# Kernel tuning notes

Hardware: AMD Instinct MI355X
Metric: run time of the kernel (lower is better)

The kernel has to match this reference:

```python
import jax, jax.numpy as jnp
import numpy as np

N = 131072          # batch_size(64) * cycle_size(2048) total graph nodes
E = 2097152         # N * avg_degree(16) edges


def _gcn_block(x, edge_index, W_self, W_nbr, b):
    """GraphConv-style STGCN spatial block: self-transform + mean-aggregated
    neighbor transform over edge_index (gather -> segment-reduce -> scatter)."""
    src, dst = edge_index[0], edge_index[1]
    msg = jax.ops.segment_sum(x[src], dst, num_segments=N)            # [N, C_in]
    deg = jax.ops.segment_sum(jnp.ones((edge_index.shape[1],), x.dtype), dst,
                              num_segments=N)                          # [N]
    agg = msg / jnp.maximum(deg, 1.0)[:, None]
    return x @ W_self + agg @ W_nbr + b


def setup_inputs() -> dict:
    key = jax.random.key(0)
    ks = jax.random.split(key, 16)

    def lin(k, fan_in, fan_out):
        return jax.random.normal(k, (fan_in, fan_out), jnp.float32) / np.sqrt(fan_in)

    x = jax.random.normal(ks[0], (N, 16), jnp.float32)
    edge_index = jax.random.randint(ks[1], (2, E), 0, N)
    batch = jnp.zeros((N,), jnp.int64) if jax.config.jax_enable_x64 else jnp.zeros((N,), jnp.int32)

    return {
        "x": x,
        "edge_index": edge_index,
        "batch": batch,
        "W_lin": lin(ks[2], 16, 16),
        "b_lin": jnp.zeros((16,), jnp.float32),
        # block3: 16 -> 32
        "Ws3": lin(ks[3], 16, 32), "Wn3": lin(ks[4], 16, 32), "b3": jnp.zeros((32,), jnp.float32),
        # block2: 32 -> 64
        "Ws2": lin(ks[5], 32, 64), "Wn2": lin(ks[6], 32, 64), "b2": jnp.zeros((64,), jnp.float32),
        # block1: 64 -> 128
        "Ws1": lin(ks[7], 64, 128), "Wn1": lin(ks[8], 64, 128), "b1": jnp.zeros((128,), jnp.float32),
    }


def reference(x, edge_index, batch, W_lin, b_lin,
              Ws3, Wn3, b3, Ws2, Wn2, b2, Ws1, Wn1, b1):
    h = x @ W_lin + b_lin                                   # Linear(16,16)
    h = jax.nn.relu(_gcn_block(h, edge_index, Ws3, Wn3, b3))   # 16 -> 32
    h = jax.nn.relu(_gcn_block(h, edge_index, Ws2, Wn2, b2))   # 32 -> 64
    h = jax.nn.sigmoid(_gcn_block(h, edge_index, Ws1, Wn1, b1))  # 64 -> 128
    return h
```

## Files before the change

kernel.cpp:

```cpp
#include <hip/hip_runtime.h>
#include <cmath>


typedef __attribute__((ext_vector_type(8))) _Float16 half8;
typedef __attribute__((ext_vector_type(4))) float floatx4;

#define NBUCKET 512
#define BUCKET_SHIFT 8

__global__ __launch_bounds__(256) void bucket_hist_kernel(
    const int* __restrict__ dst, int* __restrict__ bcnt, int E, int EPB, int nblk) {
    __shared__ int lh[NBUCKET];
    for (int i = threadIdx.x; i < NBUCKET; i += 256) lh[i] = 0;
    __syncthreads();
    int base = blockIdx.x * EPB;
    int end  = min(base + EPB, E);
    for (int i = base + threadIdx.x; i < end; i += 256)
        atomicAdd(&lh[dst[i] >> BUCKET_SHIFT], 1);
    __syncthreads();
    for (int i = threadIdx.x; i < NBUCKET; i += 256)
        bcnt[i * nblk + blockIdx.x] = lh[i];
}

__global__ void scan1_kernel(const int* __restrict__ in, int* __restrict__ out,
                             int* __restrict__ bsum) {
    __shared__ int s[256];
    int i = blockIdx.x * 256 + threadIdx.x;
    int v = in[i];
    s[threadIdx.x] = v;
    __syncthreads();
    for (int off = 1; off < 256; off <<= 1) {
        int t = (threadIdx.x >= off) ? s[threadIdx.x - off] : 0;
        __syncthreads();
        s[threadIdx.x] += t;
        __syncthreads();
    }
    out[i] = s[threadIdx.x] - v;
    if (threadIdx.x == 255) bsum[blockIdx.x] = s[255];
}

__global__ void scan2_kernel(int* __restrict__ bsum, int NB) {
    extern __shared__ int s2[];
    int v = (threadIdx.x < NB) ? bsum[threadIdx.x] : 0;
    s2[threadIdx.x] = v;
    __syncthreads();
    for (int off = 1; off < NB; off <<= 1) {
        int t = (threadIdx.x >= off) ? s2[threadIdx.x - off] : 0;
        __syncthreads();
        s2[threadIdx.x] += t;
        __syncthreads();
    }
    if (threadIdx.x < NB) bsum[threadIdx.x] = s2[threadIdx.x] - v;
}

__global__ void scan3_kernel(int* __restrict__ out, const int* __restrict__ bsum) {
    int i = blockIdx.x * 256 + threadIdx.x;
    out[i] += bsum[blockIdx.x];
}

__global__ __launch_bounds__(256) void partition_kernel(
    const int* __restrict__ src, const int* __restrict__ dst,
    const int* __restrict__ bofs, int2* __restrict__ part,
    int E, int EPB, int nblk) {
    __shared__ int cur[NBUCKET];
    for (int i = threadIdx.x; i < NBUCKET; i += 256)
        cur[i] = bofs[i * nblk + blockIdx.x];
    __syncthreads();
    int base = blockIdx.x * EPB;
    int end  = min(base + EPB, E);
    for (int i = base + threadIdx.x; i < end; i += 256) {
        int d = dst[i];
        int p = atomicAdd(&cur[d >> BUCKET_SHIFT], 1);
        part[p] = make_int2(src[i], d);
    }
}

__global__ __launch_bounds__(256) void local_csr_kernel(
    const int* __restrict__ bofs, const int2* __restrict__ part,
    int* __restrict__ row_ptr, int* __restrict__ csr_src,
    int N, int E, int nblk, int sh) {
    __shared__ int cnt2[256 * 8];
    __shared__ int s[256];
    const int u      = blockIdx.x;
    const int node0  = u << BUCKET_SHIFT;
    const int bstart = bofs[(size_t)u * nblk];
    const int bend   = (u + 1 < gridDim.x) ? bofs[(size_t)(u + 1) * nblk] : E;
    const int tid = threadIdx.x;

    for (int k = tid; k < 256 * 8; k += 256) cnt2[k] = 0;
    __syncthreads();
    for (int i = bstart + tid; i < bend; i += 256) {
        int2 e = part[i];
        atomicAdd(&cnt2[((e.y - node0) << 3) + (e.x >> sh)], 1);
    }
    __syncthreads();

    int loc[8];
    int tot = 0;
#pragma unroll
    for (int k = 0; k < 8; k++) { loc[k] = tot; tot += cnt2[tid * 8 + k]; }
    s[tid] = tot;
    __syncthreads();
    for (int off = 1; off < 256; off <<= 1) {
        int t2 = (tid >= off) ? s[tid - off] : 0;
        __syncthreads();
        s[tid] += t2;
        __syncthreads();
    }
    int excl  = s[tid] - tot;
    int rbase = bstart + excl;
    if (node0 + tid < N) row_ptr[node0 + tid] = rbase;
    if (u == 0 && tid == 0) row_ptr[N] = E;
#pragma unroll
    for (int k = 0; k < 8; k++) cnt2[tid * 8 + k] = rbase + loc[k];
    __syncthreads();
    for (int i = bstart + tid; i < bend; i += 256) {
        int2 e = part[i];
        int p = atomicAdd(&cnt2[((e.y - node0) << 3) + (e.x >> sh)], 1);
        csr_src[p] = e.x;
    }
}

__global__ void wt_kernel(const float* __restrict__ Ws, const float* __restrict__ Wn,
                          _Float16* __restrict__ Wt, int CI, int NOUT) {
    int K = 2 * CI;
    int idx = blockIdx.x * 256 + threadIdx.x;
    if (idx >= NOUT * K) return;
    int n = idx / K, k = idx - n * K;
    float v = (k < CI) ? Ws[(size_t)k * NOUT + n] : Wn[(size_t)(k - CI) * NOUT + n];
    Wt[idx] = (_Float16)v;
}

__global__ void lin16_kernel(const float* __restrict__ x, const float* __restrict__ W,
                             const float* __restrict__ b, _Float16* __restrict__ h, int N) {
    __shared__ float sW[256];
    __shared__ float sb[16];
    sW[threadIdx.x] = W[threadIdx.x];
    if (threadIdx.x < 16) sb[threadIdx.x] = b[threadIdx.x];
    __syncthreads();
    int n = blockIdx.x * blockDim.x + threadIdx.x;
    if (n >= N) return;
    const float4* xr = (const float4*)(x + (size_t)n * 16);
    float4 x0 = xr[0], x1 = xr[1], x2 = xr[2], x3 = xr[3];
    float xi[16] = {x0.x, x0.y, x0.z, x0.w, x1.x, x1.y, x1.z, x1.w,
                    x2.x, x2.y, x2.z, x2.w, x3.x, x3.y, x3.z, x3.w};
    float o[16];
#pragma unroll
    for (int j = 0; j < 16; j++) o[j] = sb[j];
#pragma unroll
    for (int k = 0; k < 16; k++) {
        float xv = xi[k];
#pragma unroll
        for (int j = 0; j < 16; j++) o[j] += xv * sW[k * 16 + j];
    }
    half8 h0v, h1v;
#pragma unroll
    for (int j = 0; j < 8; j++) { h0v[j] = (_Float16)o[j]; h1v[j] = (_Float16)o[j + 8]; }
    half8* hr = (half8*)(h + (size_t)n * 16);
    hr[0] = h0v;
    hr[1] = h1v;
}

template <int C>
__global__ __launch_bounds__(256) void gather_kernel(
    const int* __restrict__ row_ptr, const int* __restrict__ csr_src,
    const _Float16* __restrict__ h, _Float16* __restrict__ agg, int N) {
    constexpr int GP = C / 16;
    int t = blockIdx.x * 256 + threadIdx.x;
    if (t >= N * GP) return;
    int n = t / GP;
    int g = t - n * GP;
    const int beg = row_ptr[n];
    const int end = row_ptr[n + 1];
    const size_t goff = (size_t)g * 16;

    float a[16];
#pragma unroll
    for (int i = 0; i < 16; i++) a[i] = 0.f;

    int j = beg;
    for (; j + 4 <= end; j += 4) {
        int i0 = __builtin_nontemporal_load(csr_src + j + 0);
        int i1 = __builtin_nontemporal_load(csr_src + j + 1);
        int i2 = __builtin_nontemporal_load(csr_src + j + 2);
        int i3 = __builtin_nontemporal_load(csr_src + j + 3);
        const half8* r0 = (const half8*)(h + (size_t)i0 * C + goff);
        const half8* r1 = (const half8*)(h + (size_t)i1 * C + goff);
        const half8* r2 = (const half8*)(h + (size_t)i2 * C + goff);
        const half8* r3 = (const half8*)(h + (size_t)i3 * C + goff);
        half8 v0l = r0[0], v0h = r0[1];
        half8 v1l = r1[0], v1h = r1[1];
        half8 v2l = r2[0], v2h = r2[1];
        half8 v3l = r3[0], v3h = r3[1];
#pragma unroll
        for (int i = 0; i < 8; i++) {
            a[i]     += ((float)v0l[i] + (float)v1l[i]) + ((float)v2l[i] + (float)v3l[i]);
            a[i + 8] += ((float)v0h[i] + (float)v1h[i]) + ((float)v2h[i] + (float)v3h[i]);
        }
    }
    if (j < end) {
        const int last = end - 1;
        int i0 = csr_src[j];
        int i1 = csr_src[min(j + 1, last)];
        int i2 = csr_src[min(j + 2, last)];
        int i3 = csr_src[min(j + 3, last)];
        const half8* r0 = (const half8*)(h + (size_t)i0 * C + goff);
        const half8* r1 = (const half8*)(h + (size_t)i1 * C + goff);
        const half8* r2 = (const half8*)(h + (size_t)i2 * C + goff);
        const half8* r3 = (const half8*)(h + (size_t)i3 * C + goff);
        half8 v0l = r0[0], v0h = r0[1];
        half8 v1l = r1[0], v1h = r1[1];
        half8 v2l = r2[0], v2h = r2[1];
        half8 v3l = r3[0], v3h = r3[1];
        float w1 = (j + 1 < end) ? 1.f : 0.f;
        float w2 = (j + 2 < end) ? 1.f : 0.f;
        float w3 = (j + 3 < end) ? 1.f : 0.f;
#pragma unroll
        for (int i = 0; i < 8; i++) {
            a[i]     += ((float)v0l[i] + w1 * (float)v1l[i]) + (w2 * (float)v2l[i] + w3 * (float)v3l[i]);
            a[i + 8] += ((float)v0h[i] + w1 * (float)v1h[i]) + (w2 * (float)v2h[i] + w3 * (float)v3h[i]);
        }
    }

    float inv = 1.0f / fmaxf((float)(end - beg), 1.0f);
    half8 rl, rh;
#pragma unroll
    for (int i = 0; i < 8; i++) { rl[i] = (_Float16)(a[i] * inv); rh[i] = (_Float16)(a[i + 8] * inv); }
    half8* ap = (half8*)(agg + (size_t)n * C + goff);
    __builtin_nontemporal_store(rl, ap);
    __builtin_nontemporal_store(rh, ap + 1);
}

template <int CI, int NOUT, int ACT, bool OUT_F16>
__global__ __launch_bounds__(256) void mfma_gemm_kernel(
    const _Float16* __restrict__ hbuf, const _Float16* __restrict__ abuf,
    const _Float16* __restrict__ Wt,
    const float* __restrict__ bias, void* __restrict__ outp, int N)
{
    constexpr int K   = 2 * CI;
    constexpr int KS  = K / 32;
    constexpr int CT  = NOUT / 16;
    constexpr int LDW = K + 8;
    __shared__ _Float16 Bt[NOUT * LDW];

    const int tid = threadIdx.x;
    for (int idx = tid; idx < NOUT * (K / 8); idx += 256) {
        int n  = idx / (K / 8);
        int kq = idx - n * (K / 8);
        *(half8*)&Bt[n * LDW + kq * 8] = *(const half8*)(Wt + (size_t)n * K + kq * 8);
    }
    __syncthreads();

    const int wave = tid >> 6;
    const int lane = tid & 63;
    const int m    = lane & 15;
    const int quad = lane >> 4;
    const int row0 = blockIdx.x * 64 + wave * 16;
    const size_t row = (size_t)(row0 + m);

    floatx4 acc[CT];
#pragma unroll
    for (int c = 0; c < CT; c++) acc[c] = (floatx4){0.f, 0.f, 0.f, 0.f};

#pragma unroll
    for (int s = 0; s < KS; s++) {
        int k8 = s * 32 + quad * 8;
        const _Float16* Ap = (k8 < CI) ? (hbuf + row * CI + k8)
                                       : (abuf + row * CI + (k8 - CI));
        half8 a = *(const half8*)Ap;
#pragma unroll
        for (int c = 0; c < CT; c++) {
            half8 b = *(const half8*)&Bt[(c * 16 + m) * LDW + k8];
            acc[c] = __builtin_amdgcn_mfma_f32_16x16x32_f16(a, b, acc[c], 0, 0, 0);
        }
    }

#pragma unroll
    for (int c = 0; c < CT; c++) {
        int col = c * 16 + m;
        float bv = bias[col];
#pragma unroll
        for (int j = 0; j < 4; j++) {
            int orow = row0 + quad * 4 + j;
            float v = acc[c][j] + bv;
            if (ACT == 0) v = fmaxf(v, 0.0f);
            else          v = 1.0f / (1.0f + __expf(-v));
            if (OUT_F16) ((_Float16*)outp)[(size_t)orow * NOUT + col] = (_Float16)v;
            else         ((float*)outp)[(size_t)orow * NOUT + col] = v;
        }
    }
}

extern "C" void kernel_launch(void* const* d_in, const int* in_sizes, int n_in,
                              void* d_out, int out_size, void* d_ws, size_t ws_size,
                              hipStream_t stream) {
    const float* x     = (const float*)d_in[0];
    const int*   ei    = (const int*)d_in[1];
    const float* W_lin = (const float*)d_in[3];
    const float* b_lin = (const float*)d_in[4];
    const float* Ws3   = (const float*)d_in[5];
    const float* Wn3   = (const float*)d_in[6];
    const float* b3    = (const float*)d_in[7];
    const float* Ws2   = (const float*)d_in[8];
    const float* Wn2   = (const float*)d_in[9];
    const float* b2    = (const float*)d_in[10];
    const float* Ws1   = (const float*)d_in[11];
    const float* Wn1   = (const float*)d_in[12];
    const float* b1    = (const float*)d_in[13];
    float* out = (float*)d_out;

    const int N = in_sizes[0] / 16;
    const int E = in_sizes[1] / 2;
    const int* src = ei;
    const int* dst = ei + E;

    const int NBLK = 512;
    const int EPB  = (E + NBLK - 1) / NBLK;
    const int M    = NBUCKET * NBLK;
    const int NB2  = M / 256;
    int LOGN = 0; while ((1 << (LOGN + 1)) <= N) LOGN++;
    const int SH = (LOGN >= 3) ? (LOGN - 3) : 0;

    int* wsi = (int*)d_ws;
    int* row_ptr = wsi;
    size_t B0 = ((size_t)(N + 1) + 3) & ~(size_t)3;
    int* bcnt = wsi + B0;
    int* bofs = bcnt + M;
    int* bsum = bofs + M;
    size_t C0 = (B0 + 2 * (size_t)M + (size_t)NB2 + 3) & ~(size_t)3;
    int* csr_src = wsi + C0;
    size_t P0 = (C0 + (size_t)E + 3) & ~(size_t)3;
    int2* part = (int2*)(wsi + P0);
    size_t H0 = (P0 + 2 * (size_t)E + 3) & ~(size_t)3;
    _Float16* regA = (_Float16*)(wsi + H0);
    _Float16* regB = regA + (size_t)64 * N;
    _Float16* Wt1  = regB + (size_t)64 * N;
    _Float16* Wt2  = Wt1 + 16384;
    _Float16* Wt3  = Wt2 + 4096;

    _Float16* h0    = regA;
    _Float16* agg16 = regA + (size_t)16 * N;
    _Float16* h2    = regA;
    _Float16* h3    = regB;
    _Float16* agg32 = regB + (size_t)32 * N;
    _Float16* agg64 = regB;

    const int BLK = 256;

    wt_kernel<<<(32 * 32 + 255) / 256, 256, 0, stream>>>(Ws3, Wn3, Wt3, 16, 32);
    wt_kernel<<<(64 * 64 + 255) / 256, 256, 0, stream>>>(Ws2, Wn2, Wt2, 32, 64);
    wt_kernel<<<(128 * 128 + 255) / 256, 256, 0, stream>>>(Ws1, Wn1, Wt1, 64, 128);

    bucket_hist_kernel<<<NBLK, 256, 0, stream>>>(dst, bcnt, E, EPB, NBLK);
    scan1_kernel<<<NB2, 256, 0, stream>>>(bcnt, bofs, bsum);
    scan2_kernel<<<1, NB2, NB2 * sizeof(int), stream>>>(bsum, NB2);
    scan3_kernel<<<NB2, 256, 0, stream>>>(bofs, bsum);
    partition_kernel<<<NBLK, 256, 0, stream>>>(src, dst, bofs, part, E, EPB, NBLK);
    local_csr_kernel<<<NBUCKET, 256, 0, stream>>>(bofs, part, row_ptr, csr_src, N, E, NBLK, SH);

    lin16_kernel<<<(N + BLK - 1) / BLK, BLK, 0, stream>>>(x, W_lin, b_lin, h0, N);

    gather_kernel<16><<<((size_t)N * 1 + BLK - 1) / BLK, BLK, 0, stream>>>(row_ptr, csr_src, h0, agg16, N);
    mfma_gemm_kernel<16, 32, 0, true><<<N / 64, 256, 0, stream>>>(h0, agg16, Wt3, b3, h3, N);

    gather_kernel<32><<<((size_t)N * 2 + BLK - 1) / BLK, BLK, 0, stream>>>(row_ptr, csr_src, h3, agg32, N);
    mfma_gemm_kernel<32, 64, 0, true><<<N / 64, 256, 0, stream>>>(h3, agg32, Wt2, b2, h2, N);

    gather_kernel<64><<<((size_t)N * 4 + BLK - 1) / BLK, BLK, 0, stream>>>(row_ptr, csr_src, h2, agg64, N);
    mfma_gemm_kernel<64, 128, 1, false><<<N / 64, 256, 0, stream>>>(h2, agg64, Wt1, b1, out, N);
}
```

Before: 342.9 us.

## Quantize post-ReLU activations to uint8 for neighbor gathers in blocks 2 and 1

Tracks the global max of the ReLU outputs in the GEMM epilogue with atomics. A new kernel quantizes the fp16 activations to 8-bit with that per-tensor scale, and the gathers read the 8-bit copy with integer accumulation. This halves the bytes moved by the random-access gathers of the 32- and 64-channel layers, at the cost of an extra quantization pass, atomics, and lower precision in the aggregated features.

```diff
diff --git a/kernel.cpp b/kernel.cpp
--- a/kernel.cpp
+++ b/kernel.cpp
@@ -7,6 +7,8 @@
 
 #define NBUCKET 512
 #define BUCKET_SHIFT 8
+
+__global__ void init_scales_kernel(int* __restrict__ g) { g[0] = 0; g[1] = 0; }
 
 __global__ __launch_bounds__(256) void bucket_hist_kernel(
     const int* __restrict__ dst, int* __restrict__ bcnt, int E, int EPB, int nblk) {
@@ -231,17 +233,123 @@
     __builtin_nontemporal_store(rh, ap + 1);
 }
 
-template <int CI, int NOUT, int ACT, bool OUT_F16>
+__global__ __launch_bounds__(256) void quant_kernel(
+    const _Float16* __restrict__ h, const int* __restrict__ maxbits,
+    unsigned char* __restrict__ q, int total16) {
+    int t = blockIdx.x * 256 + threadIdx.x;
+    if (t >= total16) return;
+    float M = __int_as_float(*maxbits);
+    float inv = (M > 1e-20f) ? 255.0f / M : 0.0f;
+    const half8* hp = (const half8*)(h + (size_t)t * 16);
+    half8 v0 = hp[0], v1 = hp[1];
+    unsigned int dw[4] = {0u, 0u, 0u, 0u};
+#pragma unroll
+    for (int i = 0; i < 8; i++) {
+        unsigned int b = (unsigned int)((float)v0[i] * inv + 0.5f);
+        if (b > 255u) b = 255u;
+        dw[i >> 2] |= b << ((i & 3) * 8);
+    }
+#pragma unroll
+    for (int i = 0; i < 8; i++) {
+        unsigned int b = (unsigned int)((float)v1[i] * inv + 0.5f);
+        if (b > 255u) b = 255u;
+        dw[2 + (i >> 2)] |= b << ((i & 3) * 8);
+    }
+    uint4 o; o.x = dw[0]; o.y = dw[1]; o.z = dw[2]; o.w = dw[3];
+    *(uint4*)(q + (size_t)t * 16) = o;
+}
+
+#define ACC4(d, o)                                 \
+    { unsigned int _d = (d);                        \
+      a[(o)]     += _d & 0xffu;                     \
+      a[(o) + 1] += (_d >> 8) & 0xffu;              \
+      a[(o) + 2] += (_d >> 16) & 0xffu;             \
+      a[(o) + 3] += _d >> 24; }
+#define ACC4W(d, w, o)                              \
+    { unsigned int _d = (d); int _w = (w);          \
+      a[(o)]     += _w * (int)(_d & 0xffu);         \
+      a[(o) + 1] += _w * (int)((_d >> 8) & 0xffu);  \
+      a[(o) + 2] += _w * (int)((_d >> 16) & 0xffu); \
+      a[(o) + 3] += _w * (int)(_d >> 24); }
+
+template <int C>
+__global__ __launch_bounds__(256) void gatherq_kernel(
+    const int* __restrict__ row_ptr, const int* __restrict__ csr_src,
+    const unsigned char* __restrict__ hq, const int* __restrict__ maxbits,
+    _Float16* __restrict__ agg, int N) {
+    constexpr int GP = C / 16;
+    int t = blockIdx.x * 256 + threadIdx.x;
+    if (t >= N * GP) return;
+    int n = t / GP;
+    int g = t & (GP - 1);
+    const int beg = row_ptr[n];
+    const int end = row_ptr[n + 1];
+    const size_t goff = (size_t)g * 16;
+
+    int a[16];
+#pragma unroll
+    for (int i = 0; i < 16; i++) a[i] = 0;
+
+    int j = beg;
+    for (; j + 4 <= end; j += 4) {
+        int i0 = __builtin_nontemporal_load(csr_src + j + 0);
+        int i1 = __builtin_nontemporal_load(csr_src + j + 1);
+        int i2 = __builtin_nontemporal_load(csr_src + j + 2);
+        int i3 = __builtin_nontemporal_load(csr_src + j + 3);
+        uint4 q0 = *(const uint4*)(hq + (size_t)i0 * C + goff);
+        uint4 q1 = *(const uint4*)(hq + (size_t)i1 * C + goff);
+        uint4 q2 = *(const uint4*)(hq + (size_t)i2 * C + goff);
+        uint4 q3 = *(const uint4*)(hq + (size_t)i3 * C + goff);
+        ACC4(q0.x, 0) ACC4(q0.y, 4) ACC4(q0.z, 8) ACC4(q0.w, 12)
+        ACC4(q1.x, 0) ACC4(q1.y, 4) ACC4(q1.z, 8) ACC4(q1.w, 12)
+        ACC4(q2.x, 0) ACC4(q2.y, 4) ACC4(q2.z, 8) ACC4(q2.w, 12)
+        ACC4(q3.x, 0) ACC4(q3.y, 4) ACC4(q3.z, 8) ACC4(q3.w, 12)
+    }
+    if (j < end) {
+        const int last = end - 1;
+        int i0 = csr_src[j];
+        int i1 = csr_src[min(j + 1, last)];
+        int i2 = csr_src[min(j + 2, last)];
+        int i3 = csr_src[min(j + 3, last)];
+        uint4 q0 = *(const uint4*)(hq + (size_t)i0 * C + goff);
+        uint4 q1 = *(const uint4*)(hq + (size_t)i1 * C + goff);
+        uint4 q2 = *(const uint4*)(hq + (size_t)i2 * C + goff);
+        uint4 q3 = *(const uint4*)(hq + (size_t)i3 * C + goff);
+        int w1 = (j + 1 < end) ? 1 : 0;
+        int w2 = (j + 2 < end) ? 1 : 0;
+        int w3 = (j + 3 < end) ? 1 : 0;
+        ACC4(q0.x, 0) ACC4(q0.y, 4) ACC4(q0.z, 8) ACC4(q0.w, 12)
+        ACC4W(q1.x, w1, 0) ACC4W(q1.y, w1, 4) ACC4W(q1.z, w1, 8) ACC4W(q1.w, w1, 12)
+        ACC4W(q2.x, w2, 0) ACC4W(q2.y, w2, 4) ACC4W(q2.z, w2, 8) ACC4W(q2.w, w2, 12)
+        ACC4W(q3.x, w3, 0) ACC4W(q3.y, w3, 4) ACC4W(q3.z, w3, 8) ACC4W(q3.w, w3, 12)
+    }
+
+    float M = __int_as_float(*maxbits);
+    float sc = (M * (1.0f / 255.0f)) / fmaxf((float)(end - beg), 1.0f);
+    half8 rl, rh;
+#pragma unroll
+    for (int i = 0; i < 8; i++) {
+        rl[i] = (_Float16)((float)a[i] * sc);
+        rh[i] = (_Float16)((float)a[i + 8] * sc);
+    }
+    half8* ap = (half8*)(agg + (size_t)n * C + goff);
+    __builtin_nontemporal_store(rl, ap);
+    __builtin_nontemporal_store(rh, ap + 1);
+}
+
+template <int CI, int NOUT, int ACT, bool OUT_F16, bool TRACKMAX>
 __global__ __launch_bounds__(256) void mfma_gemm_kernel(
     const _Float16* __restrict__ hbuf, const _Float16* __restrict__ abuf,
     const _Float16* __restrict__ Wt,
-    const float* __restrict__ bias, void* __restrict__ outp, int N)
+    const float* __restrict__ bias, void* __restrict__ outp,
+    int* __restrict__ maxbits, int N)
 {
     constexpr int K   = 2 * CI;
     constexpr int KS  = K / 32;
     constexpr int CT  = NOUT / 16;
     constexpr int LDW = K + 8;
     __shared__ _Float16 Bt[NOUT * LDW];
+    __shared__ int smax;
 
     const int tid = threadIdx.x;
     for (int idx = tid; idx < NOUT * (K / 8); idx += 256) {
@@ -249,6 +357,7 @@
         int kq = idx - n * (K / 8);
         *(half8*)&Bt[n * LDW + kq * 8] = *(const half8*)(Wt + (size_t)n * K + kq * 8);
     }
+    if (TRACKMAX && tid == 0) smax = 0;
     __syncthreads();
 
     const int wave = tid >> 6;
@@ -275,6 +384,7 @@
         }
     }
 
+    float tmax = 0.0f;
 #pragma unroll
     for (int c = 0; c < CT; c++) {
         int col = c * 16 + m;
@@ -285,9 +395,15 @@
             float v = acc[c][j] + bv;
             if (ACT == 0) v = fmaxf(v, 0.0f);
             else          v = 1.0f / (1.0f + __expf(-v));
+            if (TRACKMAX) tmax = fmaxf(tmax, v);
             if (OUT_F16) ((_Float16*)outp)[(size_t)orow * NOUT + col] = (_Float16)v;
             else         ((float*)outp)[(size_t)orow * NOUT + col] = v;
         }
+    }
+    if (TRACKMAX) {
+        atomicMax(&smax, __float_as_int(tmax));
+        __syncthreads();
+        if (tid == 0) atomicMax(maxbits, smax);
     }
 }
 
@@ -327,7 +443,8 @@
     int* bcnt = wsi + B0;
     int* bofs = bcnt + M;
     int* bsum = bofs + M;
-    size_t C0 = (B0 + 2 * (size_t)M + (size_t)NB2 + 3) & ~(size_t)3;
+    int* gmax = bsum + NB2;
+    size_t C0 = (B0 + 2 * (size_t)M + (size_t)NB2 + 2 + 3) & ~(size_t)3;
     int* csr_src = wsi + C0;
     size_t P0 = (C0 + (size_t)E + 3) & ~(size_t)3;
     int2* part = (int2*)(wsi + P0);
@@ -345,7 +462,12 @@
     _Float16* agg32 = regB + (size_t)32 * N;
     _Float16* agg64 = regB;
 
+    unsigned char* h3q = (unsigned char*)part;
+    unsigned char* h2q = (unsigned char*)part + (size_t)32 * N;
+
     const int BLK = 256;
+
+    init_scales_kernel<<<1, 1, 0, stream>>>(gmax);
 
     wt_kernel<<<(32 * 32 + 255) / 256, 256, 0, stream>>>(Ws3, Wn3, Wt3, 16, 32);
     wt_kernel<<<(64 * 64 + 255) / 256, 256, 0, stream>>>(Ws2, Wn2, Wt2, 32, 64);
@@ -360,12 +482,19 @@
 
     lin16_kernel<<<(N + BLK - 1) / BLK, BLK, 0, stream>>>(x, W_lin, b_lin, h0, N);
 
-    gather_kernel<16><<<((size_t)N * 1 + BLK - 1) / BLK, BLK, 0, stream>>>(row_ptr, csr_src, h0, agg16, N);
-    mfma_gemm_kernel<16, 32, 0, true><<<N / 64, 256, 0, stream>>>(h0, agg16, Wt3, b3, h3, N);
-
-    gather_kernel<32><<<((size_t)N * 2 + BLK - 1) / BLK, BLK, 0, stream>>>(row_ptr, csr_src, h3, agg32, N);
-    mfma_gemm_kernel<32, 64, 0, true><<<N / 64, 256, 0, stream>>>(h3, agg32, Wt2, b2, h2, N);
-
-    gather_kernel<64><<<((size_t)N * 4 + BLK - 1) / BLK, BLK, 0, stream>>>(row_ptr, csr_src, h2, agg64, N);
-    mfma_gemm_kernel<64, 128, 1, false><<<N / 64, 256, 0, stream>>>(h2, agg64, Wt1, b1, out, N);
-}
+    gather_kernel<16><<<((size_t)N + BLK - 1) / BLK, BLK, 0, stream>>>(row_ptr, csr_src, h0, agg16, N);
+    mfma_gemm_kernel<16, 32, 0, true, true><<<N / 64, 256, 0, stream>>>(
+        h0, agg16, Wt3, b3, h3, gmax + 0, N);
+
+    quant_kernel<<<(N * 32 / 16 + BLK - 1) / BLK, BLK, 0, stream>>>(h3, gmax + 0, h3q, N * 32 / 16);
+    gatherq_kernel<32><<<((size_t)N * 2 + BLK - 1) / BLK, BLK, 0, stream>>>(
+        row_ptr, csr_src, h3q, gmax + 0, agg32, N);
+    mfma_gemm_kernel<32, 64, 0, true, true><<<N / 64, 256, 0, stream>>>(
+        h3, agg32, Wt2, b2, h2, gmax + 1, N);
+
+    quant_kernel<<<(N * 64 / 16 + BLK - 1) / BLK, BLK, 0, stream>>>(h2, gmax + 1, h2q, N * 64 / 16);
+    gatherq_kernel<64><<<((size_t)N * 4 + BLK - 1) / BLK, BLK, 0, stream>>>(
+        row_ptr, csr_src, h2q, gmax + 1, agg64, N);
+    mfma_gemm_kernel<64, 128, 1, false, false><<<N / 64, 256, 0, stream>>>(
+        h2, agg64, Wt1, b1, out, nullptr, N);
+}
```

Result: slower. 353.8 us (+3.2%).
